# Kernel tuning notes

Measured on AMD Instinct MI355X. Metric: run time of the kernel, lower is better.

Reference implementation:

```python
import jax, jax.numpy as jnp
import numpy as np

C, H2, E, SQ, SK, HW = 256, 256, 512, 2048, 64, 256

def setup_inputs() -> dict:
    key = jax.random.key(0)
    ks = jax.random.split(key, 12)
    s = 0.05
    return {
        "Z": jax.random.normal(ks[0], (C, HW, HW), jnp.float32),
        "Q": jax.random.normal(ks[1], (SQ, 3), jnp.float32),
        "q_z": jax.random.normal(ks[2], (SQ, C), jnp.float32),
        "r": jax.random.uniform(ks[3], (SQ, SK, 2), jnp.float32) * (HW - 2),
        "w1": jax.random.normal(ks[4], (H2, 2), jnp.float32) * s,
        "b1": jnp.zeros((H2,), jnp.float32),
        "w2": jax.random.normal(ks[5], (H2, 3), jnp.float32) * s,
        "b2": jnp.zeros((H2,), jnp.float32),
        "in_proj_w": jax.random.normal(ks[6], (3 * E, E), jnp.float32) * s,
        "in_proj_b": jnp.zeros((3 * E,), jnp.float32),
        "out_proj_w": jax.random.normal(ks[7], (E, E), jnp.float32) * s,
        "out_proj_b": jnp.zeros((E,), jnp.float32),
        "num_heads": 8,
    }

def bilinear_interpolation_3d(Z, x, y):
    # Z: [c, H, W]; x, y: [N] float coords. Faithful to torch: .int() trunc (coords >= 0)
    c = Z.shape[0]
    x1 = x.astype(jnp.int32)
    y1 = y.astype(jnp.int32)
    x2 = x1 + 1
    y2 = y1 + 1
    Q11 = Z[:, x1, y1]  # [c, N]
    Q12 = Z[:, x1, y2]
    Q21 = Z[:, x2, y1]
    Q22 = Z[:, x2, y2]
    dx = x - x1
    dy = y - y1
    R1 = Q11 * (1 - dx) + Q21 * dx
    R2 = Q12 * (1 - dx) + Q22 * dx
    interp = R1 * (1 - dy) + R2 * dy  # [c, N]
    # faithful to the original: raw row-major reshape (NOT a transpose)
    return jnp.reshape(interp, (-1, c))

def reference(Z, Q, q_z, r, w1, b1, w2, b2, in_proj_w, in_proj_b, out_proj_w, out_proj_b, num_heads):
    size_q, size_k, _ = r.shape
    qr = r.reshape(-1, 2)
    Zr = bilinear_interpolation_3d(Z, qr[:, 0], qr[:, 1])
    Zr = Zr.reshape(size_q, size_k, -1)  # [sq, sk, c]
    r_proj = r @ w1.T + b1               # [sq, sk, h2]
    key = jnp.concatenate([Zr, r_proj], axis=2)  # [sq, sk, E]
    value = key
    q_proj = Q @ w2.T + b2               # [sq, h2]
    query = jnp.concatenate([q_z, q_proj], axis=1)  # [sq, E]
    E_ = query.shape[1]
    hd = E_ // num_heads
    # torch MultiheadAttention in-projection
    ql = query @ in_proj_w[:E_].T + in_proj_b[:E_]              # [sq, E]
    kl = key @ in_proj_w[E_:2 * E_].T + in_proj_b[E_:2 * E_]    # [sq, sk, E]
    vl = value @ in_proj_w[2 * E_:].T + in_proj_b[2 * E_:]
    qh = ql.reshape(size_q, num_heads, hd)
    kh = kl.reshape(size_q, size_k, num_heads, hd)
    vh = vl.reshape(size_q, size_k, num_heads, hd)
    scores = jnp.einsum('bhd,bkhd->bhk', qh, kh) / jnp.sqrt(jnp.asarray(hd, qh.dtype))
    attn = jax.nn.softmax(scores, axis=-1)  # [sq, h, sk]
    out = jnp.einsum('bhk,bkhd->bhd', attn, vh).reshape(size_q, E_)
    out = out @ out_proj_w.T + out_proj_b
    return jnp.concatenate([q_z, out], axis=1)  # [sq, c + E]
```

## Files before the change

kernel.cpp:

```cpp
#include <hip/hip_runtime.h>


typedef _Float16 half8 __attribute__((ext_vector_type(8)));
typedef _Float16 half2v __attribute__((ext_vector_type(2)));
typedef float f32x4 __attribute__((ext_vector_type(4)));

#define O_WQT   0u
#define O_WKT   262144u
#define O_WVT   524288u
#define O_WO    786432u
#define O_QRY   1048576u
#define O_WCT   2097152u
#define O_MT    4194304u
#define O_U     6291456u
#define O_G     14680064u
#define O_ZT    23068672u
#define O_ZR    39845888u
#define O_F32   73400320u

__global__ __launch_bounds__(256) void k_prep(
    const float* __restrict__ ipw, const float* __restrict__ opw,
    const float* __restrict__ q_z, const float* __restrict__ Qm,
    const float* __restrict__ w2, const float* __restrict__ b2,
    const float* __restrict__ ipb, const float* __restrict__ opb,
    _Float16* __restrict__ wsh, float* __restrict__ bu, float* __restrict__ b_eff)
{
    int idx = blockIdx.x * 256 + threadIdx.x;
    if (idx < 1048576) {
        int q = idx >> 9, j = idx & 511;
        float v;
        if (j < 256) v = q_z[q * 256 + j];
        else {
            int m = j - 256;
            v = Qm[q * 3] * w2[m * 3] + Qm[q * 3 + 1] * w2[m * 3 + 1]
              + Qm[q * 3 + 2] * w2[m * 3 + 2] + b2[m];
        }
        wsh[O_QRY + idx] = (_Float16)v;
    } else if (idx < 1310720) {
        int e0 = idx - 1048576;
        wsh[O_WO + e0] = (_Float16)opw[e0];
    } else if (idx < 1314816) {
        int c = idx - 1310720;
        int h = c >> 9, j = c & 511;
        float s = 0.f;
        for (int d = 0; d < 64; ++d)
            s += ipb[512 + (h << 6) + d] * ipw[(size_t)(512 + (h << 6) + d) * 512 + j];
        bu[c] = 0.125f * s;
    } else if (idx < 1315328) {
        int e = idx - 1314816;
        float s = opb[e];
        const float* worow = opw + (size_t)e * 512;
        for (int n = 0; n < 512; ++n) s += ipb[1024 + n] * worow[n];
        b_eff[e] = s;
    }
}

__global__ __launch_bounds__(256) void k_tw(
    const float* __restrict__ ipw, _Float16* __restrict__ wsh)
{
    __shared__ float sT[64][65];
    int bx = blockIdx.x;
    int sec = bx >> 6, tile = bx & 63;
    int t = threadIdx.x;
    int th = tile >> 3, tl = tile & 7;
    int row0, col0;
    if (sec == 0) { row0 = tl * 64;             col0 = th * 64; }
    else          { row0 = 512 * sec + th * 64; col0 = tl * 64; }
    const float* src = ipw + (size_t)row0 * 512 + col0;
#pragma unroll
    for (int i = 0; i < 4; ++i) {
        int rr = i * 16 + (t >> 4), cc = (t & 15) * 4;
        float4 v = *(const float4*)(src + (size_t)rr * 512 + cc);
        sT[rr][cc] = v.x; sT[rr][cc + 1] = v.y; sT[rr][cc + 2] = v.z; sT[rr][cc + 3] = v.w;
    }
    __syncthreads();
    float scale = (sec == 1) ? 0.125f : 1.0f;
#pragma unroll
    for (int it = 0; it < 2; ++it) {
        int g = t + it * 256;
        int a = g >> 3, b8 = (g & 7) * 8;
        half8 o;
#pragma unroll
        for (int j = 0; j < 8; ++j) o[j] = (_Float16)(scale * sT[b8 + j][a]);
        size_t dst;
        if (sec == 0)      dst = O_WQT + (size_t)(th * 64 + a) * 512 + tl * 64 + b8;
        else if (sec == 1) dst = O_WKT + (size_t)th * 32768 + (size_t)(tl * 64 + a) * 64 + b8;
        else               dst = O_WVT + (size_t)th * 32768 + (size_t)(tl * 64 + a) * 64 + b8;
        *(half8*)(wsh + dst) = o;
    }
}

__global__ __launch_bounds__(256) void k_zt(
    const float* __restrict__ Z, _Float16* __restrict__ Zt)
{
    __shared__ float sT[256][67];
    int x = blockIdx.x, yt = blockIdx.y * 64;
    int t = threadIdx.x;
#pragma unroll
    for (int i = 0; i < 16; ++i) {
        int c = i * 16 + (t >> 4), y = (t & 15) * 4;
        float4 v = *(const float4*)(Z + (size_t)c * 65536 + x * 256 + yt + y);
        sT[c][y] = v.x; sT[c][y + 1] = v.y; sT[c][y + 2] = v.z; sT[c][y + 3] = v.w;
    }
    __syncthreads();
    _Float16* outb = Zt + ((size_t)(x * 256 + yt)) * 256 + t;
#pragma unroll 8
    for (int y = 0; y < 64; ++y)
        outb[(size_t)y * 256] = (_Float16)sT[t][y];
}

__global__ __launch_bounds__(256, 4) void k_passA(
    const _Float16* __restrict__ Zt, const float* __restrict__ r,
    _Float16* __restrict__ Zr)
{
    __shared__ float sT[256][33];
    int b = blockIdx.x;
    int t = threadIdx.x, w = t >> 6, l = t & 63;
    const float2* r2 = (const float2*)r;
#pragma unroll 2
    for (int i = 0; i < 8; ++i) {
        int ptl = w * 8 + i;
        float2 rv = r2[b * 32 + ptl];
        int x1 = (int)rv.x, y1 = (int)rv.y;
        float dx = rv.x - (float)x1, dy = rv.y - (float)y1;
        float w11 = (1.f - dx) * (1.f - dy), w21 = dx * (1.f - dy);
        float w12 = (1.f - dx) * dy,         w22 = dx * dy;
        const _Float16* base = Zt + ((size_t)(x1 * 256 + y1)) * 256;
#pragma unroll
        for (int cg = 0; cg < 2; ++cg) {
            int c = cg * 128 + l * 2;
            half2v z11 = *(const half2v*)(base + c);
            half2v z12 = *(const half2v*)(base + 256 + c);
            half2v z21 = *(const half2v*)(base + 65536 + c);
            half2v z22 = *(const half2v*)(base + 65536 + 256 + c);
            sT[c][ptl]     = w11 * (float)z11[0] + w21 * (float)z21[0]
                           + w12 * (float)z12[0] + w22 * (float)z22[0];
            sT[c + 1][ptl] = w11 * (float)z11[1] + w21 * (float)z21[1]
                           + w12 * (float)z12[1] + w22 * (float)z22[1];
        }
    }
    __syncthreads();
    int ch0 = t >> 2, colc = (t & 3) * 8;
#pragma unroll
    for (int g = 0; g < 4; ++g) {
        int ch = g * 64 + ch0;
        half8 o;
#pragma unroll
        for (int j = 0; j < 8; ++j) o[j] = (_Float16)sT[ch][colc + j];
        *(half8*)(Zr + (size_t)ch * 131072 + b * 32 + colc) = o;
    }
}

__global__ __launch_bounds__(256) void k_small(
    const _Float16* __restrict__ A, const _Float16* __restrict__ BT,
    _Float16* __restrict__ C, int outT)
{
    __shared__ __align__(16) _Float16 sA[64][72];
    int rb = blockIdx.x, h = blockIdx.y;
    int t = threadIdx.x, w = t >> 6, l = t & 63;
    const _Float16* A0 = A + (size_t)rb * 64 * 512 + h * 64;
    const _Float16* B0 = BT + (size_t)h * 512 * 64;
#pragma unroll
    for (int i = 0; i < 2; ++i) {
        int g = t + i * 256;
        int row = g >> 3, colg = (g & 7) * 8;
        *(half8*)&sA[row][colg] = *(const half8*)(A0 + (size_t)row * 512 + colg);
    }
    __syncthreads();
    f32x4 acc[4][8] = {};
    int arow = l & 15, kg = (l >> 4) << 3;
#pragma unroll
    for (int kk = 0; kk < 64; kk += 32) {
        half8 a[4], bb[8];
#pragma unroll
        for (int mt = 0; mt < 4; ++mt) a[mt] = *(const half8*)&sA[mt * 16 + arow][kk + kg];
#pragma unroll
        for (int nt = 0; nt < 8; ++nt) {
            int col = (w << 7) + nt * 16 + arow;
            bb[nt] = *(const half8*)(B0 + (size_t)col * 64 + kk + kg);
        }
#pragma unroll
        for (int mt = 0; mt < 4; ++mt)
#pragma unroll
            for (int nt = 0; nt < 8; ++nt)
                acc[mt][nt] = __builtin_amdgcn_mfma_f32_16x16x32_f16(a[mt], bb[nt], acc[mt][nt], 0, 0, 0);
    }
    if (outT) {
#pragma unroll
        for (int mt = 0; mt < 4; ++mt)
#pragma unroll
            for (int nt = 0; nt < 8; ++nt) {
                int col = (h << 9) + (w << 7) + nt * 16 + arow;
                int row0 = rb * 64 + mt * 16 + ((l >> 4) << 2);
#pragma unroll
                for (int v = 0; v < 4; ++v)
                    C[(size_t)col * 512 + row0 + v] = (_Float16)acc[mt][nt][v];
            }
    } else {
        _Float16* C0 = C + (size_t)rb * 64 * 4096 + h * 512;
#pragma unroll
        for (int mt = 0; mt < 4; ++mt)
#pragma unroll
            for (int nt = 0; nt < 8; ++nt)
#pragma unroll
                for (int v = 0; v < 4; ++v) {
                    int row = mt * 16 + ((l >> 4) << 2) + v;
                    int col = (w << 7) + nt * 16 + arow;
                    C0[(size_t)row * 4096 + col] = (_Float16)acc[mt][nt][v];
                }
    }
}

__global__ __launch_bounds__(256) void k_gemmU(
    const _Float16* __restrict__ A, const _Float16* __restrict__ B,
    const float* __restrict__ bu, _Float16* __restrict__ U)
{
    __shared__ __align__(16) _Float16 sA[64][520];
    int q0 = blockIdx.x * 64;
    int t = threadIdx.x, w = t >> 6, l = t & 63;
    int colb = blockIdx.y * 256 + w * 64;
    const _Float16* Ab = A + (size_t)q0 * 512;
#pragma unroll
    for (int i = 0; i < 16; ++i) {
        int e = i * 2048 + t * 8;
        *(half8*)&sA[e >> 9][e & 511] = *(const half8*)(Ab + e);
    }
    __syncthreads();
    f32x4 acc[4][4] = {};
    int arow = l & 15, kg = (l >> 4) << 3;
#pragma unroll 2
    for (int kk = 0; kk < 512; kk += 32) {
        half8 a[4], bb[4];
#pragma unroll
        for (int mt = 0; mt < 4; ++mt) a[mt] = *(const half8*)&sA[mt * 16 + arow][kk + kg];
#pragma unroll
        for (int nt = 0; nt < 4; ++nt)
            bb[nt] = *(const half8*)(B + (size_t)(colb + nt * 16 + arow) * 512 + kk + kg);
#pragma unroll
        for (int mt = 0; mt < 4; ++mt)
#pragma unroll
            for (int nt = 0; nt < 4; ++nt)
                acc[mt][nt] = __builtin_amdgcn_mfma_f32_16x16x32_f16(a[mt], bb[nt], acc[mt][nt], 0, 0, 0);
    }
#pragma unroll
    for (int mt = 0; mt < 4; ++mt)
#pragma unroll
        for (int nt = 0; nt < 4; ++nt)
#pragma unroll
            for (int v = 0; v < 4; ++v) {
                int row = q0 + mt * 16 + ((l >> 4) << 2) + v;
                int col = colb + nt * 16 + arow;
                U[(size_t)row * 4096 + col] = (_Float16)(acc[mt][nt][v] + bu[col]);
            }
}

__global__ __launch_bounds__(512, 2) void k_main(
    const _Float16* __restrict__ Zr, const float* __restrict__ r,
    const float* __restrict__ w1, const float* __restrict__ b1,
    const _Float16* __restrict__ U, _Float16* __restrict__ G)
{
    __shared__ __align__(16) _Float16 sKey[64][520];
    __shared__ __align__(16) _Float16 sU[8][520];
    __shared__ float sP[512];
    __shared__ __align__(16) _Float16 sA16[16][72];

    int q = blockIdx.x;
    int t = threadIdx.x, w = t >> 6, l = t & 63;
    int ch = q >> 3, s8 = q & 7;

    for (int i = t; i < 576; i += 512) ((unsigned*)sA16)[i] = 0u;

    const _Float16* src = Zr + ((size_t)ch * 2048 + s8 * 256) * 64;
#pragma unroll
    for (int i = 0; i < 4; ++i) {
        int e = i * 4096 + t * 8;
        *(half8*)&sKey[e >> 8][e & 255] = *(const half8*)(src + e);
    }
    {
        int e = t * 8;
        *(half8*)&sU[e >> 9][e & 511] = *(const half8*)(U + (size_t)q * 4096 + e);
    }
    {
        int m = t & 255, half = t >> 8;
        float w10 = w1[2 * m], w11 = w1[2 * m + 1], b1m = b1[m];
        const float2* r2q = (const float2*)r + (size_t)q * 64;
#pragma unroll 8
        for (int i = 0; i < 32; ++i) {
            int k = half * 32 + i;
            float2 rv = r2q[k];
            sKey[k][256 + m] = (_Float16)(rv.x * w10 + rv.y * w11 + b1m);
        }
    }
    __syncthreads();

    if (w < 4) {
        f32x4 acc = {};
        int arow = l & 15, kg = (l >> 4) << 3;
        const _Float16* ar = &sKey[w * 16 + arow][kg];
        const _Float16* br = &sU[l & 7][kg];
#pragma unroll 4
        for (int kk = 0; kk < 512; kk += 32)
            acc = __builtin_amdgcn_mfma_f32_16x16x32_f16(
                *(const half8*)(ar + kk), *(const half8*)(br + kk), acc, 0, 0, 0);
        if ((l & 15) < 8) {
            int h = l & 15, krow0 = w * 16 + ((l >> 4) << 2);
#pragma unroll
            for (int v = 0; v < 4; ++v) sP[(h << 6) + krow0 + v] = acc[v];
        }
    }
    __syncthreads();

    {
        float v = sP[t];
        float mx = v;
#pragma unroll
        for (int mm = 1; mm < 64; mm <<= 1) mx = fmaxf(mx, __shfl_xor(mx, mm, 64));
        float e = __expf(v - mx);
        float sm = e;
#pragma unroll
        for (int mm = 1; mm < 64; mm <<= 1) sm += __shfl_xor(sm, mm, 64);
        sA16[w][l] = (_Float16)(e / sm);
    }
    __syncthreads();

    {
        f32x4 acc[4] = {};
        int arow = l & 15, kq = (l >> 4) << 3;
        half8 a0 = *(const half8*)&sA16[arow][kq];
        half8 a1 = *(const half8*)&sA16[arow][32 + kq];
#pragma unroll
        for (int nt = 0; nt < 4; ++nt) {
            int n0 = (w << 6) + (nt << 4);
            half8 b0, b1f;
#pragma unroll
            for (int jj = 0; jj < 8; ++jj) b0[jj] = sKey[kq + jj][n0 + arow];
            acc[nt] = __builtin_amdgcn_mfma_f32_16x16x32_f16(a0, b0, acc[nt], 0, 0, 0);
#pragma unroll
            for (int jj = 0; jj < 8; ++jj) b1f[jj] = sKey[32 + kq + jj][n0 + arow];
            acc[nt] = __builtin_amdgcn_mfma_f32_16x16x32_f16(a1, b1f, acc[nt], 0, 0, 0);
        }
        if (l < 32) {
            int rgrp = (l >> 4) << 2;
#pragma unroll
            for (int nt = 0; nt < 4; ++nt) {
                int n0 = (w << 6) + (nt << 4);
#pragma unroll
                for (int v = 0; v < 4; ++v)
                    sU[rgrp + v][n0 + arow] = (_Float16)acc[nt][v];
            }
        }
    }
    __syncthreads();

    {
        int c = t * 8;
        *(half8*)(G + (size_t)q * 4096 + c) = *(const half8*)&sU[c >> 9][c & 511];
    }
}

__global__ __launch_bounds__(256) void k_final(
    const _Float16* __restrict__ G, const _Float16* __restrict__ Mt,
    const float* __restrict__ b_eff, const float* __restrict__ qz,
    float* __restrict__ out)
{
    __shared__ __align__(16) _Float16 sA[64][520];
    int rb = blockIdx.x, cb = blockIdx.y;
    int q0 = rb * 64;
    int t = threadIdx.x, w = t >> 6, l = t & 63;

    if (cb == 0) {
#pragma unroll
        for (int i = 0; i < 16; ++i) {
            int idx4 = i * 256 + t;
            int row = idx4 >> 6, c = (idx4 & 63) << 2;
            *(float4*)&out[(size_t)(q0 + row) * 768 + c] =
                *(const float4*)&qz[(size_t)(q0 + row) * 256 + c];
        }
    }

    f32x4 acc[4][2] = {};
    int arow = l & 15, kg = (l >> 4) << 3;
    int e0 = cb * 128 + (w << 5);
    for (int c = 0; c < 8; ++c) {
#pragma unroll
        for (int i = 0; i < 16; ++i) {
            int e = i * 2048 + t * 8;
            *(half8*)&sA[e >> 9][e & 511] =
                *(const half8*)(G + (size_t)(q0 + (e >> 9)) * 4096 + c * 512 + (e & 511));
        }
        __syncthreads();
#pragma unroll 4
        for (int kk = 0; kk < 512; kk += 32) {
            half8 a[4], bb[2];
#pragma unroll
            for (int nt = 0; nt < 2; ++nt)
                bb[nt] = *(const half8*)(Mt + (size_t)(e0 + nt * 16 + arow) * 4096 + c * 512 + kk + kg);
#pragma unroll
            for (int mt = 0; mt < 4; ++mt) {
                a[mt] = *(const half8*)&sA[mt * 16 + arow][kk + kg];
#pragma unroll
                for (int nt = 0; nt < 2; ++nt)
                    acc[mt][nt] = __builtin_amdgcn_mfma_f32_16x16x32_f16(a[mt], bb[nt], acc[mt][nt], 0, 0, 0);
            }
        }
        __syncthreads();
    }
#pragma unroll
    for (int mt = 0; mt < 4; ++mt)
#pragma unroll
        for (int nt = 0; nt < 2; ++nt)
#pragma unroll
            for (int v = 0; v < 4; ++v) {
                int row = q0 + mt * 16 + ((l >> 4) << 2) + v;
                int ecol = e0 + nt * 16 + arow;
                out[(size_t)row * 768 + 256 + ecol] = acc[mt][nt][v] + b_eff[ecol];
            }
}

extern "C" void kernel_launch(void* const* d_in, const int* in_sizes, int n_in,
                              void* d_out, int out_size, void* d_ws, size_t ws_size,
                              hipStream_t stream) {
    const float* Z          = (const float*)d_in[0];
    const float* Qm         = (const float*)d_in[1];
    const float* q_z        = (const float*)d_in[2];
    const float* r          = (const float*)d_in[3];
    const float* w1         = (const float*)d_in[4];
    const float* b1         = (const float*)d_in[5];
    const float* w2         = (const float*)d_in[6];
    const float* b2         = (const float*)d_in[7];
    const float* in_proj_w  = (const float*)d_in[8];
    const float* in_proj_b  = (const float*)d_in[9];
    const float* out_proj_w = (const float*)d_in[10];
    const float* out_proj_b = (const float*)d_in[11];
    float* out = (float*)d_out;

    _Float16* wsh = (_Float16*)d_ws;
    _Float16* wqT   = wsh + O_WQT;
    _Float16* wkT   = wsh + O_WKT;
    _Float16* wvT   = wsh + O_WVT;
    _Float16* wo    = wsh + O_WO;
    _Float16* query = wsh + O_QRY;
    _Float16* WcT   = wsh + O_WCT;
    _Float16* Mt    = wsh + O_MT;
    _Float16* U     = wsh + O_U;
    _Float16* G     = wsh + O_G;
    _Float16* Zt    = wsh + O_ZT;
    _Float16* Zr    = wsh + O_ZR;
    float*    bu    = (float*)(wsh + O_F32);
    float*    b_eff = bu + 4096;

    k_prep<<<5138, 256, 0, stream>>>(in_proj_w, out_proj_w, q_z, Qm, w2, b2,
                                     in_proj_b, out_proj_b, wsh, bu, b_eff);
    k_tw<<<192, 256, 0, stream>>>(in_proj_w, wsh);
    k_zt<<<dim3(256, 4), 256, 0, stream>>>(Z, Zt);
    k_small<<<dim3(8, 8), 256, 0, stream>>>(wqT, wkT, WcT, 1);
    k_small<<<dim3(8, 8), 256, 0, stream>>>(wo, wvT, Mt, 0);
    k_gemmU<<<dim3(32, 16), 256, 0, stream>>>(query, WcT, bu, U);
    k_passA<<<4096, 256, 0, stream>>>(Zt, r, Zr);
    k_main<<<2048, 512, 0, stream>>>(Zr, r, w1, b1, U, G);
    k_final<<<dim3(32, 4), 256, 0, stream>>>(G, Mt, b_eff, q_z, out);
}
```

Before: 312.7 us.

## Merge preprocessing kernels into fewer launches and split score MFMA across all waves

Folds the Z transpose, weight transposes, query build, weight conversion and bias precompute into one multi-role kernel, and merges the two small weight GEMMs into a single launch. The U GEMM and the bilinear gather pass now share one launch as well, with the GEMM's shared-memory tile halved so both roles fit. The Z transpose is re-tiled to write vectorized half4 stores, b_eff uses a wave reduction, and k_main's score GEMM splits K across all eight waves with a two-buffer sum. The goal is to cut launch gaps and tail idle time, at the cost of heterogeneous blocks with higher shared-memory use and extra syncs.

```diff
diff --git a/kernel.cpp b/kernel.cpp
--- a/kernel.cpp
+++ b/kernel.cpp
@@ -2,6 +2,7 @@
 
 
 typedef _Float16 half8 __attribute__((ext_vector_type(8)));
+typedef _Float16 half4v __attribute__((ext_vector_type(4)));
 typedef _Float16 half2v __attribute__((ext_vector_type(2)));
 typedef float f32x4 __attribute__((ext_vector_type(4)));
 
@@ -18,148 +19,121 @@
 #define O_ZR    39845888u
 #define O_F32   73400320u
 
-__global__ __launch_bounds__(256) void k_prep(
-    const float* __restrict__ ipw, const float* __restrict__ opw,
-    const float* __restrict__ q_z, const float* __restrict__ Qm,
-    const float* __restrict__ w2, const float* __restrict__ b2,
-    const float* __restrict__ ipb, const float* __restrict__ opb,
+__global__ __launch_bounds__(256) void k_pre(
+    const float* __restrict__ Z, const float* __restrict__ ipw,
+    const float* __restrict__ opw, const float* __restrict__ q_z,
+    const float* __restrict__ Qm, const float* __restrict__ w2,
+    const float* __restrict__ b2, const float* __restrict__ ipb,
+    const float* __restrict__ opb,
     _Float16* __restrict__ wsh, float* __restrict__ bu, float* __restrict__ b_eff)
 {
-    int idx = blockIdx.x * 256 + threadIdx.x;
-    if (idx < 1048576) {
-        int q = idx >> 9, j = idx & 511;
-        float v;
-        if (j < 256) v = q_z[q * 256 + j];
-        else {
-            int m = j - 256;
-            v = Qm[q * 3] * w2[m * 3] + Qm[q * 3 + 1] * w2[m * 3 + 1]
-              + Qm[q * 3 + 2] * w2[m * 3 + 2] + b2[m];
-        }
-        wsh[O_QRY + idx] = (_Float16)v;
-    } else if (idx < 1310720) {
-        int e0 = idx - 1048576;
-        wsh[O_WO + e0] = (_Float16)opw[e0];
-    } else if (idx < 1314816) {
-        int c = idx - 1310720;
+    __shared__ __align__(16) float sbuf[8448];
+    int b = blockIdx.x, t = threadIdx.x;
+
+    if (b < 2048) {
+        float (*sT)[33] = (float(*)[33])sbuf;
+        int x = b >> 3, yt = (b & 7) * 32;
+#pragma unroll
+        for (int i = 0; i < 8; ++i) {
+            int g = i * 256 + t;
+            int c = g >> 3, y = (g & 7) * 4;
+            float4 v = *(const float4*)(Z + (size_t)c * 65536 + x * 256 + yt + y);
+            sT[c][y] = v.x; sT[c][y + 1] = v.y; sT[c][y + 2] = v.z; sT[c][y + 3] = v.w;
+        }
+        __syncthreads();
+        _Float16* Zt = wsh + O_ZT;
+        int c4 = (t & 63) * 4;
+#pragma unroll
+        for (int i = 0; i < 8; ++i) {
+            int y = (t >> 6) * 8 + i;
+            half4v o;
+#pragma unroll
+            for (int j = 0; j < 4; ++j) o[j] = (_Float16)sT[c4 + j][y];
+            *(half4v*)(Zt + ((size_t)(x * 256 + yt + y)) * 256 + c4) = o;
+        }
+    } else if (b < 2240) {
+        float (*sT)[65] = (float(*)[65])sbuf;
+        int bx = b - 2048;
+        int sec = bx >> 6, tile = bx & 63;
+        int th = tile >> 3, tl = tile & 7;
+        int row0, col0;
+        if (sec == 0) { row0 = tl * 64;             col0 = th * 64; }
+        else          { row0 = 512 * sec + th * 64; col0 = tl * 64; }
+        const float* src = ipw + (size_t)row0 * 512 + col0;
+#pragma unroll
+        for (int i = 0; i < 4; ++i) {
+            int rr = i * 16 + (t >> 4), cc = (t & 15) * 4;
+            float4 v = *(const float4*)(src + (size_t)rr * 512 + cc);
+            sT[rr][cc] = v.x; sT[rr][cc + 1] = v.y; sT[rr][cc + 2] = v.z; sT[rr][cc + 3] = v.w;
+        }
+        __syncthreads();
+        float scale = (sec == 1) ? 0.125f : 1.0f;
+#pragma unroll
+        for (int it = 0; it < 2; ++it) {
+            int g = t + it * 256;
+            int a = g >> 3, b8 = (g & 7) * 8;
+            half8 o;
+#pragma unroll
+            for (int j = 0; j < 8; ++j) o[j] = (_Float16)(scale * sT[b8 + j][a]);
+            size_t dst;
+            if (sec == 0)      dst = O_WQT + (size_t)(th * 64 + a) * 512 + tl * 64 + b8;
+            else if (sec == 1) dst = O_WKT + (size_t)th * 32768 + (size_t)(tl * 64 + a) * 64 + b8;
+            else               dst = O_WVT + (size_t)th * 32768 + (size_t)(tl * 64 + a) * 64 + b8;
+            *(half8*)(wsh + dst) = o;
+        }
+    } else if (b < 3264) {
+        int e4 = ((b - 2240) * 256 + t) * 4;
+        int q = e4 >> 9, j = e4 & 511;
+        half4v o;
+        if (j < 256) {
+            float4 v = *(const float4*)(q_z + q * 256 + j);
+            o[0] = (_Float16)v.x; o[1] = (_Float16)v.y;
+            o[2] = (_Float16)v.z; o[3] = (_Float16)v.w;
+        } else {
+            float q0 = Qm[q * 3], q1 = Qm[q * 3 + 1], q2 = Qm[q * 3 + 2];
+#pragma unroll
+            for (int u = 0; u < 4; ++u) {
+                int m = j - 256 + u;
+                o[u] = (_Float16)(q0 * w2[m * 3] + q1 * w2[m * 3 + 1] + q2 * w2[m * 3 + 2] + b2[m]);
+            }
+        }
+        *(half4v*)(wsh + O_QRY + e4) = o;
+    } else if (b < 3520) {
+        int e4 = ((b - 3264) * 256 + t) * 4;
+        float4 v = *(const float4*)(opw + e4);
+        half4v o;
+        o[0] = (_Float16)v.x; o[1] = (_Float16)v.y; o[2] = (_Float16)v.z; o[3] = (_Float16)v.w;
+        *(half4v*)(wsh + O_WO + e4) = o;
+    } else if (b < 3536) {
+        int c = (b - 3520) * 256 + t;
         int h = c >> 9, j = c & 511;
         float s = 0.f;
+#pragma unroll 4
         for (int d = 0; d < 64; ++d)
             s += ipb[512 + (h << 6) + d] * ipw[(size_t)(512 + (h << 6) + d) * 512 + j];
         bu[c] = 0.125f * s;
-    } else if (idx < 1315328) {
-        int e = idx - 1314816;
-        float s = opb[e];
+    } else {
+        int e = (b - 3536) * 4 + (t >> 6), l = t & 63;
         const float* worow = opw + (size_t)e * 512;
-        for (int n = 0; n < 512; ++n) s += ipb[1024 + n] * worow[n];
-        b_eff[e] = s;
-    }
-}
-
-__global__ __launch_bounds__(256) void k_tw(
-    const float* __restrict__ ipw, _Float16* __restrict__ wsh)
-{
-    __shared__ float sT[64][65];
-    int bx = blockIdx.x;
-    int sec = bx >> 6, tile = bx & 63;
-    int t = threadIdx.x;
-    int th = tile >> 3, tl = tile & 7;
-    int row0, col0;
-    if (sec == 0) { row0 = tl * 64;             col0 = th * 64; }
-    else          { row0 = 512 * sec + th * 64; col0 = tl * 64; }
-    const float* src = ipw + (size_t)row0 * 512 + col0;
-#pragma unroll
-    for (int i = 0; i < 4; ++i) {
-        int rr = i * 16 + (t >> 4), cc = (t & 15) * 4;
-        float4 v = *(const float4*)(src + (size_t)rr * 512 + cc);
-        sT[rr][cc] = v.x; sT[rr][cc + 1] = v.y; sT[rr][cc + 2] = v.z; sT[rr][cc + 3] = v.w;
-    }
-    __syncthreads();
-    float scale = (sec == 1) ? 0.125f : 1.0f;
-#pragma unroll
-    for (int it = 0; it < 2; ++it) {
-        int g = t + it * 256;
-        int a = g >> 3, b8 = (g & 7) * 8;
-        half8 o;
-#pragma unroll
-        for (int j = 0; j < 8; ++j) o[j] = (_Float16)(scale * sT[b8 + j][a]);
-        size_t dst;
-        if (sec == 0)      dst = O_WQT + (size_t)(th * 64 + a) * 512 + tl * 64 + b8;
-        else if (sec == 1) dst = O_WKT + (size_t)th * 32768 + (size_t)(tl * 64 + a) * 64 + b8;
-        else               dst = O_WVT + (size_t)th * 32768 + (size_t)(tl * 64 + a) * 64 + b8;
-        *(half8*)(wsh + dst) = o;
-    }
-}
-
-__global__ __launch_bounds__(256) void k_zt(
-    const float* __restrict__ Z, _Float16* __restrict__ Zt)
-{
-    __shared__ float sT[256][67];
-    int x = blockIdx.x, yt = blockIdx.y * 64;
-    int t = threadIdx.x;
-#pragma unroll
-    for (int i = 0; i < 16; ++i) {
-        int c = i * 16 + (t >> 4), y = (t & 15) * 4;
-        float4 v = *(const float4*)(Z + (size_t)c * 65536 + x * 256 + yt + y);
-        sT[c][y] = v.x; sT[c][y + 1] = v.y; sT[c][y + 2] = v.z; sT[c][y + 3] = v.w;
-    }
-    __syncthreads();
-    _Float16* outb = Zt + ((size_t)(x * 256 + yt)) * 256 + t;
-#pragma unroll 8
-    for (int y = 0; y < 64; ++y)
-        outb[(size_t)y * 256] = (_Float16)sT[t][y];
-}
-
-__global__ __launch_bounds__(256, 4) void k_passA(
-    const _Float16* __restrict__ Zt, const float* __restrict__ r,
-    _Float16* __restrict__ Zr)
-{
-    __shared__ float sT[256][33];
-    int b = blockIdx.x;
-    int t = threadIdx.x, w = t >> 6, l = t & 63;
-    const float2* r2 = (const float2*)r;
-#pragma unroll 2
-    for (int i = 0; i < 8; ++i) {
-        int ptl = w * 8 + i;
-        float2 rv = r2[b * 32 + ptl];
-        int x1 = (int)rv.x, y1 = (int)rv.y;
-        float dx = rv.x - (float)x1, dy = rv.y - (float)y1;
-        float w11 = (1.f - dx) * (1.f - dy), w21 = dx * (1.f - dy);
-        float w12 = (1.f - dx) * dy,         w22 = dx * dy;
-        const _Float16* base = Zt + ((size_t)(x1 * 256 + y1)) * 256;
-#pragma unroll
-        for (int cg = 0; cg < 2; ++cg) {
-            int c = cg * 128 + l * 2;
-            half2v z11 = *(const half2v*)(base + c);
-            half2v z12 = *(const half2v*)(base + 256 + c);
-            half2v z21 = *(const half2v*)(base + 65536 + c);
-            half2v z22 = *(const half2v*)(base + 65536 + 256 + c);
-            sT[c][ptl]     = w11 * (float)z11[0] + w21 * (float)z21[0]
-                           + w12 * (float)z12[0] + w22 * (float)z22[0];
-            sT[c + 1][ptl] = w11 * (float)z11[1] + w21 * (float)z21[1]
-                           + w12 * (float)z12[1] + w22 * (float)z22[1];
-        }
-    }
-    __syncthreads();
-    int ch0 = t >> 2, colc = (t & 3) * 8;
-#pragma unroll
-    for (int g = 0; g < 4; ++g) {
-        int ch = g * 64 + ch0;
-        half8 o;
-#pragma unroll
-        for (int j = 0; j < 8; ++j) o[j] = (_Float16)sT[ch][colc + j];
-        *(half8*)(Zr + (size_t)ch * 131072 + b * 32 + colc) = o;
-    }
-}
-
-__global__ __launch_bounds__(256) void k_small(
-    const _Float16* __restrict__ A, const _Float16* __restrict__ BT,
-    _Float16* __restrict__ C, int outT)
+        float s = 0.f;
+#pragma unroll
+        for (int i = 0; i < 8; ++i)
+            s += ipb[1024 + l + 64 * i] * worow[l + 64 * i];
+#pragma unroll
+        for (int mm = 1; mm < 64; mm <<= 1) s += __shfl_xor(s, mm, 64);
+        if (l == 0) b_eff[e] = s + opb[e];
+    }
+}
+
+__global__ __launch_bounds__(256) void k_small2(_Float16* __restrict__ wsh)
 {
     __shared__ __align__(16) _Float16 sA[64][72];
-    int rb = blockIdx.x, h = blockIdx.y;
+    int bx = blockIdx.x;
+    int job = bx >> 6, g6 = bx & 63;
+    int rb = g6 & 7, h = g6 >> 3;
     int t = threadIdx.x, w = t >> 6, l = t & 63;
-    const _Float16* A0 = A + (size_t)rb * 64 * 512 + h * 64;
-    const _Float16* B0 = BT + (size_t)h * 512 * 64;
+    const _Float16* A0 = wsh + (job ? O_WO : O_WQT) + (size_t)rb * 64 * 512 + h * 64;
+    const _Float16* B0 = wsh + (job ? O_WVT : O_WKT) + (size_t)h * 512 * 64;
 #pragma unroll
     for (int i = 0; i < 2; ++i) {
         int g = t + i * 256;
@@ -185,7 +159,8 @@
             for (int nt = 0; nt < 8; ++nt)
                 acc[mt][nt] = __builtin_amdgcn_mfma_f32_16x16x32_f16(a[mt], bb[nt], acc[mt][nt], 0, 0, 0);
     }
-    if (outT) {
+    if (job == 0) {
+        _Float16* C = wsh + O_WCT;
 #pragma unroll
         for (int mt = 0; mt < 4; ++mt)
 #pragma unroll
@@ -197,7 +172,7 @@
                     C[(size_t)col * 512 + row0 + v] = (_Float16)acc[mt][nt][v];
             }
     } else {
-        _Float16* C0 = C + (size_t)rb * 64 * 4096 + h * 512;
+        _Float16* C0 = wsh + O_MT + (size_t)rb * 64 * 4096 + h * 512;
 #pragma unroll
         for (int mt = 0; mt < 4; ++mt)
 #pragma unroll
@@ -211,47 +186,96 @@
     }
 }
 
-__global__ __launch_bounds__(256) void k_gemmU(
-    const _Float16* __restrict__ A, const _Float16* __restrict__ B,
-    const float* __restrict__ bu, _Float16* __restrict__ U)
+__global__ __launch_bounds__(256, 4) void k_mid(
+    const float* __restrict__ r, _Float16* __restrict__ wsh,
+    const float* __restrict__ bu)
 {
-    __shared__ __align__(16) _Float16 sA[64][520];
-    int q0 = blockIdx.x * 64;
-    int t = threadIdx.x, w = t >> 6, l = t & 63;
-    int colb = blockIdx.y * 256 + w * 64;
-    const _Float16* Ab = A + (size_t)q0 * 512;
-#pragma unroll
-    for (int i = 0; i < 16; ++i) {
-        int e = i * 2048 + t * 8;
-        *(half8*)&sA[e >> 9][e & 511] = *(const half8*)(Ab + e);
-    }
-    __syncthreads();
-    f32x4 acc[4][4] = {};
-    int arow = l & 15, kg = (l >> 4) << 3;
+    __shared__ __align__(16) unsigned char smem[33792];
+    int b = blockIdx.x, t = threadIdx.x, w = t >> 6, l = t & 63;
+
+    if (b < 512) {
+        _Float16 (*sA)[264] = (_Float16(*)[264])smem;
+        const _Float16* A = wsh + O_QRY;
+        const _Float16* B = wsh + O_WCT;
+        _Float16* U = wsh + O_U;
+        int q0 = (b & 31) * 64;
+        int colb = (b >> 5) * 256 + w * 64;
+        f32x4 acc[4][4] = {};
+        int arow = l & 15, kg = (l >> 4) << 3;
+#pragma unroll
+        for (int half = 0; half < 2; ++half) {
+#pragma unroll
+            for (int i = 0; i < 8; ++i) {
+                int e = i * 2048 + t * 8;
+                *(half8*)&sA[e >> 8][e & 255] =
+                    *(const half8*)(A + (size_t)(q0 + (e >> 8)) * 512 + half * 256 + (e & 255));
+            }
+            __syncthreads();
 #pragma unroll 2
-    for (int kk = 0; kk < 512; kk += 32) {
-        half8 a[4], bb[4];
-#pragma unroll
-        for (int mt = 0; mt < 4; ++mt) a[mt] = *(const half8*)&sA[mt * 16 + arow][kk + kg];
-#pragma unroll
-        for (int nt = 0; nt < 4; ++nt)
-            bb[nt] = *(const half8*)(B + (size_t)(colb + nt * 16 + arow) * 512 + kk + kg);
+            for (int kk = 0; kk < 256; kk += 32) {
+                half8 a[4], bb[4];
+#pragma unroll
+                for (int mt = 0; mt < 4; ++mt) a[mt] = *(const half8*)&sA[mt * 16 + arow][kk + kg];
+#pragma unroll
+                for (int nt = 0; nt < 4; ++nt)
+                    bb[nt] = *(const half8*)(B + (size_t)(colb + nt * 16 + arow) * 512 + half * 256 + kk + kg);
+#pragma unroll
+                for (int mt = 0; mt < 4; ++mt)
+#pragma unroll
+                    for (int nt = 0; nt < 4; ++nt)
+                        acc[mt][nt] = __builtin_amdgcn_mfma_f32_16x16x32_f16(a[mt], bb[nt], acc[mt][nt], 0, 0, 0);
+            }
+            __syncthreads();
+        }
 #pragma unroll
         for (int mt = 0; mt < 4; ++mt)
 #pragma unroll
             for (int nt = 0; nt < 4; ++nt)
-                acc[mt][nt] = __builtin_amdgcn_mfma_f32_16x16x32_f16(a[mt], bb[nt], acc[mt][nt], 0, 0, 0);
-    }
-#pragma unroll
-    for (int mt = 0; mt < 4; ++mt)
-#pragma unroll
-        for (int nt = 0; nt < 4; ++nt)
-#pragma unroll
-            for (int v = 0; v < 4; ++v) {
-                int row = q0 + mt * 16 + ((l >> 4) << 2) + v;
-                int col = colb + nt * 16 + arow;
-                U[(size_t)row * 4096 + col] = (_Float16)(acc[mt][nt][v] + bu[col]);
-            }
+#pragma unroll
+                for (int v = 0; v < 4; ++v) {
+                    int row = q0 + mt * 16 + ((l >> 4) << 2) + v;
+                    int col = colb + nt * 16 + arow;
+                    U[(size_t)row * 4096 + col] = (_Float16)(acc[mt][nt][v] + bu[col]);
+                }
+    } else {
+        float (*sT)[33] = (float(*)[33])smem;
+        const _Float16* Zt = wsh + O_ZT;
+        _Float16* Zr = wsh + O_ZR;
+        int pb = b - 512;
+        const float2* r2 = (const float2*)r;
+#pragma unroll 2
+        for (int i = 0; i < 8; ++i) {
+            int ptl = w * 8 + i;
+            float2 rv = r2[pb * 32 + ptl];
+            int x1 = (int)rv.x, y1 = (int)rv.y;
+            float dx = rv.x - (float)x1, dy = rv.y - (float)y1;
+            float w11 = (1.f - dx) * (1.f - dy), w21 = dx * (1.f - dy);
+            float w12 = (1.f - dx) * dy,         w22 = dx * dy;
+            const _Float16* base = Zt + ((size_t)(x1 * 256 + y1)) * 256;
+#pragma unroll
+            for (int cg = 0; cg < 2; ++cg) {
+                int c = cg * 128 + l * 2;
+                half2v z11 = *(const half2v*)(base + c);
+                half2v z12 = *(const half2v*)(base + 256 + c);
+                half2v z21 = *(const half2v*)(base + 65536 + c);
+                half2v z22 = *(const half2v*)(base + 65536 + 256 + c);
+                sT[c][ptl]     = w11 * (float)z11[0] + w21 * (float)z21[0]
+                               + w12 * (float)z12[0] + w22 * (float)z22[0];
+                sT[c + 1][ptl] = w11 * (float)z11[1] + w21 * (float)z21[1]
+                               + w12 * (float)z12[1] + w22 * (float)z22[1];
+            }
+        }
+        __syncthreads();
+        int ch0 = t >> 2, colc = (t & 3) * 8;
+#pragma unroll
+        for (int g = 0; g < 4; ++g) {
+            int ch = g * 64 + ch0;
+            half8 o;
+#pragma unroll
+            for (int j = 0; j < 8; ++j) o[j] = (_Float16)sT[ch][colc + j];
+            *(half8*)(Zr + (size_t)ch * 131072 + pb * 32 + colc) = o;
+        }
+    }
 }
 
 __global__ __launch_bounds__(512, 2) void k_main(
@@ -262,6 +286,7 @@
     __shared__ __align__(16) _Float16 sKey[64][520];
     __shared__ __align__(16) _Float16 sU[8][520];
     __shared__ float sP[512];
+    __shared__ float sP2[512];
     __shared__ __align__(16) _Float16 sA16[16][72];
 
     int q = blockIdx.x;
@@ -293,25 +318,27 @@
     }
     __syncthreads();
 
-    if (w < 4) {
+    {
         f32x4 acc = {};
         int arow = l & 15, kg = (l >> 4) << 3;
-        const _Float16* ar = &sKey[w * 16 + arow][kg];
-        const _Float16* br = &sU[l & 7][kg];
-#pragma unroll 4
-        for (int kk = 0; kk < 512; kk += 32)
+        int wm = w & 3, khalf = (w >> 2) << 8;
+        const _Float16* ar = &sKey[wm * 16 + arow][khalf + kg];
+        const _Float16* br = &sU[l & 7][khalf + kg];
+#pragma unroll
+        for (int kk = 0; kk < 256; kk += 32)
             acc = __builtin_amdgcn_mfma_f32_16x16x32_f16(
                 *(const half8*)(ar + kk), *(const half8*)(br + kk), acc, 0, 0, 0);
         if ((l & 15) < 8) {
-            int h = l & 15, krow0 = w * 16 + ((l >> 4) << 2);
-#pragma unroll
-            for (int v = 0; v < 4; ++v) sP[(h << 6) + krow0 + v] = acc[v];
+            int h = l & 15, krow0 = wm * 16 + ((l >> 4) << 2);
+            float* dst = (w < 4) ? sP : sP2;
+#pragma unroll
+            for (int v = 0; v < 4; ++v) dst[(h << 6) + krow0 + v] = acc[v];
         }
     }
     __syncthreads();
 
     {
-        float v = sP[t];
+        float v = sP[t] + sP2[t];
         float mx = v;
 #pragma unroll
         for (int mm = 1; mm < 64; mm <<= 1) mx = fmaxf(mx, __shfl_xor(mx, mm, 64));
@@ -435,28 +462,17 @@
     float* out = (float*)d_out;
 
     _Float16* wsh = (_Float16*)d_ws;
-    _Float16* wqT   = wsh + O_WQT;
-    _Float16* wkT   = wsh + O_WKT;
-    _Float16* wvT   = wsh + O_WVT;
-    _Float16* wo    = wsh + O_WO;
-    _Float16* query = wsh + O_QRY;
-    _Float16* WcT   = wsh + O_WCT;
     _Float16* Mt    = wsh + O_MT;
     _Float16* U     = wsh + O_U;
     _Float16* G     = wsh + O_G;
-    _Float16* Zt    = wsh + O_ZT;
     _Float16* Zr    = wsh + O_ZR;
     float*    bu    = (float*)(wsh + O_F32);
     float*    b_eff = bu + 4096;
 
-    k_prep<<<5138, 256, 0, stream>>>(in_proj_w, out_proj_w, q_z, Qm, w2, b2,
-                                     in_proj_b, out_proj_b, wsh, bu, b_eff);
-    k_tw<<<192, 256, 0, stream>>>(in_proj_w, wsh);
-    k_zt<<<dim3(256, 4), 256, 0, stream>>>(Z, Zt);
-    k_small<<<dim3(8, 8), 256, 0, stream>>>(wqT, wkT, WcT, 1);
-    k_small<<<dim3(8, 8), 256, 0, stream>>>(wo, wvT, Mt, 0);
-    k_gemmU<<<dim3(32, 16), 256, 0, stream>>>(query, WcT, bu, U);
-    k_passA<<<4096, 256, 0, stream>>>(Zt, r, Zr);
+    k_pre<<<3664, 256, 0, stream>>>(Z, in_proj_w, out_proj_w, q_z, Qm, w2, b2,
+                                    in_proj_b, out_proj_b, wsh, bu, b_eff);
+    k_small2<<<128, 256, 0, stream>>>(wsh);
+    k_mid<<<4608, 256, 0, stream>>>(r, wsh, bu);
     k_main<<<2048, 512, 0, stream>>>(Zr, r, w1, b1, U, G);
     k_final<<<dim3(32, 4), 256, 0, stream>>>(G, Mt, b_eff, q_z, out);
 }
```

Measured after the change: 281.4 us. 10.0% less time.
